# Optimization experiments

Hardware: AMD Instinct MI355X
Metric: run time of the kernel (lower is better)

The kernel has to match this reference:

```python
import jax, jax.numpy as jnp
import numpy as np

B, S, D, H = 4, 2048, 1024, 16
DK = D // H
NEG = -1e9


def setup_inputs() -> dict:
    key = jax.random.key(0)
    ks = jax.random.split(key, 8)
    q = jax.random.normal(ks[0], (B, S, D), dtype=jnp.float32)
    k = jax.random.normal(ks[1], (B, S, D), dtype=jnp.float32)
    v = jax.random.normal(ks[2], (B, S, D), dtype=jnp.float32)
    # causal mask, broadcastable to [B,H,S,S]; mask==0 -> masked out
    mask = jnp.tril(jnp.ones((S, S), dtype=jnp.int32))[None, None, :, :]
    scale = 1.0 / np.sqrt(D)
    w_q = jax.random.normal(ks[3], (D, D), dtype=jnp.float32) * scale
    w_k = jax.random.normal(ks[4], (D, D), dtype=jnp.float32) * scale
    w_v = jax.random.normal(ks[5], (D, D), dtype=jnp.float32) * scale
    w_o = jax.random.normal(ks[6], (D, D), dtype=jnp.float32) * scale
    return {"q": q, "k": k, "v": v, "mask": mask,
            "w_q": w_q, "w_k": w_k, "w_v": w_v, "w_o": w_o}


def reference(q, k, v, mask, w_q, w_k, w_v, w_o):
    # projections (nn.Linear with no bias: x @ W^T)
    def proj(x, w):
        y = jnp.einsum('bsd,ed->bse', x, w)          # [B,S,D]
        return y.reshape(B, -1, H, DK).transpose(0, 2, 1, 3)  # [B,H,S,DK]
    Q, K, V = proj(q, w_q), proj(k, w_k), proj(v, w_v)
    scores = jnp.einsum('bhqd,bhkd->bhqk', Q, K) * (DK ** -0.5)  # [B,H,S,S]
    scores = jnp.where(mask == 0, NEG, scores)
    attn = jax.nn.softmax(scores, axis=-1)
    x = jnp.einsum('bhqk,bhkd->bhqd', attn, V)       # [B,H,S,DK]
    x = x.transpose(0, 2, 1, 3).reshape(B, -1, D)    # [B,S,D]
    return jnp.einsum('bsd,ed->bse', x, w_o)
```

## Files before the change

kernel.cpp:

```cpp
#include <hip/hip_runtime.h>
#include <hip/hip_bf16.h>
#include <stdint.h>

#define B_ 4
#define S_ 2048
#define D_ 1024
#define H_ 16
#define DK_ 64

typedef __hip_bfloat16 bf16;
typedef __attribute__((ext_vector_type(8))) __bf16 bf16x8;
typedef __attribute__((ext_vector_type(4))) __bf16 bf16x4;
typedef __attribute__((ext_vector_type(4))) float f32x4;
typedef __attribute__((ext_vector_type(4))) uint32_t u32x4;

#define QSCALE 0.18033688011112042f

#if defined(__has_builtin)
#if __has_builtin(__builtin_amdgcn_exp2f)
#define EXP2(x) __builtin_amdgcn_exp2f(x)
#endif
#endif
#ifndef EXP2
#define EXP2(x) exp2f(x)
#endif

__device__ __forceinline__ void async_copy16(const void* g, void* l) {
    __builtin_amdgcn_global_load_lds((const __attribute__((address_space(1))) void*)g,
                                     (__attribute__((address_space(3))) void*)l,
                                     16, 0, 0);
}

__device__ __forceinline__ bf16x8 ld8(const bf16* p) {
    return *(const bf16x8*)p;
}

__device__ __forceinline__ uint32_t pk2(float a, float b) {
    union { __bf16 h; uint16_t u; } x, y;
    x.h = (__bf16)a; y.h = (__bf16)b;
    return (uint32_t)x.u | ((uint32_t)y.u << 16);
}

__device__ __forceinline__ bf16x8 cvt8(float4 u0, float4 u1) {
    return (bf16x8){(__bf16)u0.x, (__bf16)u0.y, (__bf16)u0.z, (__bf16)u0.w,
                    (__bf16)u1.x, (__bf16)u1.y, (__bf16)u1.z, (__bf16)u1.w};
}

__device__ __forceinline__ bf16x8 transpose_p(const float* p0, const float* p1,
                                              int srcl, bool loT) {
    uint32_t x0 = pk2(p0[0], p0[1]), x1 = pk2(p0[2], p0[3]);
    uint32_t y0 = pk2(p1[0], p1[1]), y1 = pk2(p1[2], p1[3]);
    u32x4 dw;
#pragma unroll
    for (int i = 0; i < 4; i++) {
        int sl = srcl + (i >> 1) * 16;
        uint32_t vA = (uint32_t)__shfl((int)((i & 1) ? x1 : x0), sl, 64);
        uint32_t vB = (uint32_t)__shfl((int)((i & 1) ? y1 : y0), sl, 64);
        dw[i] = loT ? vA : vB;
    }
    return __builtin_bit_cast(bf16x8, dw);
}

__global__ __launch_bounds__(256) void cvtw(const float4* __restrict__ s0,
                                            const float4* __restrict__ s1,
                                            const float4* __restrict__ s2,
                                            const float4* __restrict__ s3,
                                            bf16x4* __restrict__ d0,
                                            bf16x4* __restrict__ d1,
                                            bf16x4* __restrict__ d2,
                                            bf16x4* __restrict__ d3) {
    int i = blockIdx.x * 256 + threadIdx.x;
    int seg = i >> 18;
    int j   = i & 262143;
    const float4* s = seg == 0 ? s0 : seg == 1 ? s1 : seg == 2 ? s2 : s3;
    bf16x4*       d = seg == 0 ? d0 : seg == 1 ? d1 : seg == 2 ? d2 : d3;
    float4 f = s[j];
    d[j] = (bf16x4){(__bf16)f.x, (__bf16)f.y, (__bf16)f.z, (__bf16)f.w};
}

__global__ __launch_bounds__(256) void cvtx(const float* __restrict__ s0,
                                            const float* __restrict__ s1,
                                            const float* __restrict__ s2,
                                            bf16* __restrict__ d0,
                                            bf16* __restrict__ d1,
                                            bf16* __restrict__ d2) {
    const int z = blockIdx.z;
    const float* s = z == 0 ? s0 : z == 1 ? s1 : s2;
    bf16*        d = z == 0 ? d0 : z == 1 ? d1 : d2;
    size_t i = ((size_t)blockIdx.x * 256 + threadIdx.x) * 8;
    float4 u0 = *(const float4*)(s + i);
    float4 u1 = *(const float4*)(s + i + 4);
    *(bf16x8*)(d + i) = cvt8(u0, u1);
}

__global__ __launch_bounds__(256) void gemm_qkv_bf(const bf16* __restrict__ Aq,
                                                   const bf16* __restrict__ Ak,
                                                   const bf16* __restrict__ Av,
                                                   const bf16* __restrict__ Wqb,
                                                   const bf16* __restrict__ Wkb,
                                                   const bf16* __restrict__ Wvb,
                                                   bf16* __restrict__ Oq,
                                                   bf16* __restrict__ Ok,
                                                   bf16* __restrict__ Ov) {
    __shared__ bf16 lA[128 * 32];
    __shared__ bf16 lW[128 * 32];
    const int z = blockIdx.z;
    const bf16* A = z == 0 ? Aq : z == 1 ? Ak : Av;
    const bf16* W = z == 0 ? Wqb : z == 1 ? Wkb : Wvb;
    bf16*      out = z == 0 ? Oq : z == 1 ? Ok : Ov;

    const int tid  = threadIdx.x;
    const int lane = tid & 63;
    const int quad = lane >> 4;
    const int lo   = lane & 15;
    const int wave = tid >> 6;
    const int wm   = (wave >> 1) * 64;
    const int wn   = (wave & 1) * 64;
    const int n0   = blockIdx.y * 128;
    const int m0   = blockIdx.x * 128;
    const int K    = 1024;

    f32x4 acc[4][4];
#pragma unroll
    for (int i = 0; i < 4; i++)
#pragma unroll
        for (int j = 0; j < 4; j++) acc[i][j] = (f32x4){0.f, 0.f, 0.f, 0.f};

    const int sr = tid >> 2;
    const int sc = (tid & 3) * 8;

    for (int k0 = 0; k0 < K; k0 += 32) {
        async_copy16(A + (size_t)(m0 + sr) * K + k0 + sc,       lA + sr * 32 + sc);
        async_copy16(A + (size_t)(m0 + 64 + sr) * K + k0 + sc,  lA + (64 + sr) * 32 + sc);
        async_copy16(W + (size_t)(n0 + sr) * K + k0 + sc,       lW + sr * 32 + sc);
        async_copy16(W + (size_t)(n0 + 64 + sr) * K + k0 + sc,  lW + (64 + sr) * 32 + sc);
        __syncthreads();

        bf16x8 af[4], bfr[4];
#pragma unroll
        for (int i = 0; i < 4; i++)
            af[i] = ld8(lA + (wm + i * 16 + lo) * 32 + quad * 8);
#pragma unroll
        for (int j = 0; j < 4; j++)
            bfr[j] = ld8(lW + (wn + j * 16 + lo) * 32 + quad * 8);
#pragma unroll
        for (int i = 0; i < 4; i++)
#pragma unroll
            for (int j = 0; j < 4; j++)
                acc[i][j] = __builtin_amdgcn_mfma_f32_16x16x32_bf16(af[i], bfr[j], acc[i][j], 0, 0, 0);
        __syncthreads();
    }

#pragma unroll
    for (int i = 0; i < 4; i++)
#pragma unroll
        for (int j = 0; j < 4; j++)
#pragma unroll
            for (int r = 0; r < 4; r++) {
                int m = m0 + wm + i * 16 + quad * 4 + r;
                int n = n0 + wn + j * 16 + lo;
                float val = acc[i][j][r];
                int b = m >> 11, s = m & (S_ - 1);
                int h = n >> 6, dk = n & 63;
                if (z == 0) {
                    out[((size_t)(b * H_ + h) * S_ + s) * DK_ + dk] =
                        __float2bfloat16(val * QSCALE);
                } else if (z == 1) {
                    out[((size_t)(b * H_ + h) * S_ + s) * DK_ + dk] = __float2bfloat16(val);
                } else {
                    out[((size_t)(b * H_ + h) * DK_ + dk) * S_ + s] = __float2bfloat16(val);
                }
            }
}

__global__ __launch_bounds__(256) void gemm_qkv(const float* __restrict__ Aq,
                                                const float* __restrict__ Ak,
                                                const float* __restrict__ Av,
                                                const bf16* __restrict__ Wqb,
                                                const bf16* __restrict__ Wkb,
                                                const bf16* __restrict__ Wvb,
                                                bf16* __restrict__ Oq,
                                                bf16* __restrict__ Ok,
                                                bf16* __restrict__ Ov) {
    __shared__ bf16 lA[128 * 32];
    __shared__ bf16 lW[128 * 32];
    const int z = blockIdx.z;
    const float* A = z == 0 ? Aq : z == 1 ? Ak : Av;
    const bf16*  W = z == 0 ? Wqb : z == 1 ? Wkb : Wvb;
    bf16*      out = z == 0 ? Oq : z == 1 ? Ok : Ov;

    const int tid  = threadIdx.x;
    const int lane = tid & 63;
    const int quad = lane >> 4;
    const int lo   = lane & 15;
    const int wave = tid >> 6;
    const int wm   = (wave >> 1) * 64;
    const int wn   = (wave & 1) * 64;
    const int n0   = blockIdx.y * 128;
    const int m0   = blockIdx.x * 128;
    const int K    = 1024;

    f32x4 acc[4][4];
#pragma unroll
    for (int i = 0; i < 4; i++)
#pragma unroll
        for (int j = 0; j < 4; j++) acc[i][j] = (f32x4){0.f, 0.f, 0.f, 0.f};

    const int sr = tid >> 2;
    const int sc = (tid & 3) * 8;

    for (int k0 = 0; k0 < K; k0 += 32) {
        async_copy16(W + (size_t)(n0 + sr) * K + k0 + sc,       lW + sr * 32 + sc);
        async_copy16(W + (size_t)(n0 + 64 + sr) * K + k0 + sc,  lW + (64 + sr) * 32 + sc);
        const float* a0 = A + (size_t)(m0 + sr) * K + k0 + sc;
        const float* a1 = A + (size_t)(m0 + 64 + sr) * K + k0 + sc;
        float4 u0 = *(const float4*)a0;
        float4 u1 = *(const float4*)(a0 + 4);
        float4 u2 = *(const float4*)a1;
        float4 u3 = *(const float4*)(a1 + 4);
        *(bf16x8*)(lA + sr * 32 + sc)        = cvt8(u0, u1);
        *(bf16x8*)(lA + (64 + sr) * 32 + sc) = cvt8(u2, u3);
        __syncthreads();

        bf16x8 af[4], bfr[4];
#pragma unroll
        for (int i = 0; i < 4; i++)
            af[i] = ld8(lA + (wm + i * 16 + lo) * 32 + quad * 8);
#pragma unroll
        for (int j = 0; j < 4; j++)
            bfr[j] = ld8(lW + (wn + j * 16 + lo) * 32 + quad * 8);
#pragma unroll
        for (int i = 0; i < 4; i++)
#pragma unroll
            for (int j = 0; j < 4; j++)
                acc[i][j] = __builtin_amdgcn_mfma_f32_16x16x32_bf16(af[i], bfr[j], acc[i][j], 0, 0, 0);
        __syncthreads();
    }

#pragma unroll
    for (int i = 0; i < 4; i++)
#pragma unroll
        for (int j = 0; j < 4; j++)
#pragma unroll
            for (int r = 0; r < 4; r++) {
                int m = m0 + wm + i * 16 + quad * 4 + r;
                int n = n0 + wn + j * 16 + lo;
                float val = acc[i][j][r];
                int b = m >> 11, s = m & (S_ - 1);
                int h = n >> 6, dk = n & 63;
                if (z == 0) {
                    out[((size_t)(b * H_ + h) * S_ + s) * DK_ + dk] =
                        __float2bfloat16(val * QSCALE);
                } else if (z == 1) {
                    out[((size_t)(b * H_ + h) * S_ + s) * DK_ + dk] = __float2bfloat16(val);
                } else {
                    out[((size_t)(b * H_ + h) * DK_ + dk) * S_ + s] = __float2bfloat16(val);
                }
            }
}

__global__ __launch_bounds__(256) void gemm_out(const bf16* __restrict__ A,
                                                const bf16* __restrict__ W,
                                                float* __restrict__ out) {
    __shared__ bf16 lA[128 * 32];
    __shared__ bf16 lW[128 * 32];
    const int tid  = threadIdx.x;
    const int lane = tid & 63;
    const int quad = lane >> 4;
    const int lo   = lane & 15;
    const int wave = tid >> 6;
    const int wm   = (wave >> 1) * 64;
    const int wn   = (wave & 1) * 64;
    const int n0   = blockIdx.y * 128;
    const int m0   = blockIdx.x * 128;
    const int K    = 1024;

    f32x4 acc[4][4];
#pragma unroll
    for (int i = 0; i < 4; i++)
#pragma unroll
        for (int j = 0; j < 4; j++) acc[i][j] = (f32x4){0.f, 0.f, 0.f, 0.f};

    const int sr = tid >> 2;
    const int sc = (tid & 3) * 8;

    for (int k0 = 0; k0 < K; k0 += 32) {
        async_copy16(A + (size_t)(m0 + sr) * K + k0 + sc,       lA + sr * 32 + sc);
        async_copy16(A + (size_t)(m0 + 64 + sr) * K + k0 + sc,  lA + (64 + sr) * 32 + sc);
        async_copy16(W + (size_t)(n0 + sr) * K + k0 + sc,       lW + sr * 32 + sc);
        async_copy16(W + (size_t)(n0 + 64 + sr) * K + k0 + sc,  lW + (64 + sr) * 32 + sc);
        __syncthreads();

        bf16x8 af[4], bfr[4];
#pragma unroll
        for (int i = 0; i < 4; i++)
            af[i] = ld8(lA + (wm + i * 16 + lo) * 32 + quad * 8);
#pragma unroll
        for (int j = 0; j < 4; j++)
            bfr[j] = ld8(lW + (wn + j * 16 + lo) * 32 + quad * 8);
#pragma unroll
        for (int i = 0; i < 4; i++)
#pragma unroll
            for (int j = 0; j < 4; j++)
                acc[i][j] = __builtin_amdgcn_mfma_f32_16x16x32_bf16(af[i], bfr[j], acc[i][j], 0, 0, 0);
        __syncthreads();
    }

#pragma unroll
    for (int i = 0; i < 4; i++)
#pragma unroll
        for (int j = 0; j < 4; j++)
#pragma unroll
            for (int r = 0; r < 4; r++) {
                int m = m0 + wm + i * 16 + quad * 4 + r;
                int n = n0 + wn + j * 16 + lo;
                out[(size_t)m * D_ + n] = acc[i][j][r];
            }
}

__global__ __launch_bounds__(128) void attn(const bf16* __restrict__ Q,
                                            const bf16* __restrict__ K,
                                            const bf16* __restrict__ Vt,
                                            bf16* __restrict__ X) {
    __shared__ f32x4 sO[4][4][64];
    __shared__ float sL[4][64];
    const int tid  = threadIdx.x;
    const int wid  = tid >> 6;
    const int lane = tid & 63;
    const int quad = lane >> 4;
    const int lo   = lane & 15;
    const int idx  = blockIdx.x;
    const int bh   = idx & 63;
    const int qbp  = 31 - (idx >> 6);
    const int q0   = qbp * 64;

    const bf16* Qp = Q  + (size_t)bh * S_ * DK_;
    const bf16* Kp = K  + (size_t)bh * S_ * DK_;
    const bf16* Vp = Vt + (size_t)bh * DK_ * S_;

    bf16x8 bQ[4][2];
#pragma unroll
    for (int qs = 0; qs < 4; qs++) {
        const bf16* qp = Qp + (size_t)(q0 + qs * 16 + lo) * DK_ + quad * 8;
        bQ[qs][0] = ld8(qp);
        bQ[qs][1] = ld8(qp + 32);
    }

    f32x4 out[4][4];
    float lsum[4] = {0.f, 0.f, 0.f, 0.f};
#pragma unroll
    for (int qs = 0; qs < 4; qs++)
#pragma unroll
        for (int t = 0; t < 4; t++) out[qs][t] = (f32x4){0.f, 0.f, 0.f, 0.f};

    const int NT   = 2 * qbp + 2;
    const int half = NT >> 1;
    const int it0  = wid * half;
    const int it1  = it0 + half;
    const int srcl = (quad & 1) * 32 + lo;
    const bool loT = (quad < 2);

    bf16x8 aK0, aK1, aK2, aK3;
    {
        const bf16* kn = Kp + (size_t)(it0 * 32 + lo) * DK_ + quad * 8;
        aK0 = ld8(kn); aK1 = ld8(kn + 32);
        aK2 = ld8(kn + 16 * DK_); aK3 = ld8(kn + 16 * DK_ + 32);
    }

    for (int it = it0; it < it1; ++it) {
        const int kv0 = it * 32;
        const int am = (it < 2 * qbp) ? 0 : (it == 2 * qbp ? 1 : 2);
        const int bm = (it < 2 * qbp + 1) ? 0 : 1;

        bf16x8 aV[4];
#pragma unroll
        for (int t = 0; t < 4; t++)
            aV[t] = ld8(Vp + (size_t)(t * 16 + lo) * S_ + kv0 + quad * 8);

        f32x4 st[4][2];
        __builtin_amdgcn_s_setprio(1);
#pragma unroll
        for (int qs = 0; qs < 4; qs++) {
            f32x4 t0 = (f32x4){0.f, 0.f, 0.f, 0.f};
            f32x4 t1 = (f32x4){0.f, 0.f, 0.f, 0.f};
            t0 = __builtin_amdgcn_mfma_f32_16x16x32_bf16(aK0, bQ[qs][0], t0, 0, 0, 0);
            t0 = __builtin_amdgcn_mfma_f32_16x16x32_bf16(aK1, bQ[qs][1], t0, 0, 0, 0);
            t1 = __builtin_amdgcn_mfma_f32_16x16x32_bf16(aK2, bQ[qs][0], t1, 0, 0, 0);
            t1 = __builtin_amdgcn_mfma_f32_16x16x32_bf16(aK3, bQ[qs][1], t1, 0, 0, 0);
            st[qs][0] = t0; st[qs][1] = t1;
        }
        __builtin_amdgcn_s_setprio(0);

        {
            int kvn = it + 1; if (kvn >= it1) kvn = it1 - 1;
            const bf16* kn = Kp + (size_t)(kvn * 32 + lo) * DK_ + quad * 8;
            aK0 = ld8(kn); aK1 = ld8(kn + 32);
            aK2 = ld8(kn + 16 * DK_); aK3 = ld8(kn + 16 * DK_ + 32);
        }

        bf16x8 bP[4];
#pragma unroll
        for (int pr = 0; pr < 2; pr++) {
            const int mode = pr == 0 ? am : bm;
            const int sl = pr * 2, sh = pr * 2 + 1;
            float pl0[4], pl1[4], ph0[4], ph1[4];
#pragma unroll
            for (int r = 0; r < 4; r++) {
                float el0 = EXP2(st[sl][0][r]);
                float el1 = EXP2(st[sl][1][r]);
                float eh0 = EXP2(st[sh][0][r]);
                float eh1 = EXP2(st[sh][1][r]);
                if (mode == 1) {
                    bool c = (quad * 4 + r) <= lo;
                    el0 = c ? el0 : 0.f;
                    el1 = 0.f;
                    eh1 = c ? eh1 : 0.f;
                } else if (mode == 2) {
                    el0 = 0.f; el1 = 0.f; eh0 = 0.f; eh1 = 0.f;
                }
                pl0[r] = el0; pl1[r] = el1; ph0[r] = eh0; ph1[r] = eh1;
                lsum[sl] += el0 + el1;
                lsum[sh] += eh0 + eh1;
            }
            bP[sl] = transpose_p(pl0, pl1, srcl, loT);
            bP[sh] = transpose_p(ph0, ph1, srcl, loT);
        }

        __builtin_amdgcn_s_setprio(1);
#pragma unroll
        for (int qs = 0; qs < 4; qs++)
#pragma unroll
            for (int t = 0; t < 4; t++)
                out[qs][t] = __builtin_amdgcn_mfma_f32_16x16x32_bf16(aV[t], bP[qs], out[qs][t], 0, 0, 0);
        __builtin_amdgcn_s_setprio(0);
    }

    if (wid == 1) {
#pragma unroll
        for (int qs = 0; qs < 4; qs++) {
#pragma unroll
            for (int t = 0; t < 4; t++) sO[qs][t][lane] = out[qs][t];
            sL[qs][lane] = lsum[qs];
        }
    }
    __syncthreads();
    if (wid == 0) {
        const int b = bh >> 4, h = bh & 15;
#pragma unroll
        for (int qs = 0; qs < 4; qs++) {
#pragma unroll
            for (int t = 0; t < 4; t++) {
                f32x4 p = sO[qs][t][lane];
                out[qs][t][0] += p[0]; out[qs][t][1] += p[1];
                out[qs][t][2] += p[2]; out[qs][t][3] += p[3];
            }
            float ls = lsum[qs] + sL[qs][lane];
            ls += __shfl_xor(ls, 16, 64);
            ls += __shfl_xor(ls, 32, 64);
            const float rl = 1.f / ls;
            bf16* Xp = X + (size_t)(b * S_ + q0 + qs * 16 + lo) * D_ + h * 64;
#pragma unroll
            for (int t = 0; t < 4; t++) {
                uint32_t* d = (uint32_t*)(Xp + t * 16 + quad * 4);
                d[0] = pk2(out[qs][t][0] * rl, out[qs][t][1] * rl);
                d[1] = pk2(out[qs][t][2] * rl, out[qs][t][3] * rl);
            }
        }
    }
}

extern "C" void kernel_launch(void* const* d_in, const int* in_sizes, int n_in,
                              void* d_out, int out_size, void* d_ws, size_t ws_size,
                              hipStream_t stream) {
    const float* q  = (const float*)d_in[0];
    const float* k  = (const float*)d_in[1];
    const float* v  = (const float*)d_in[2];
    const float* wq = (const float*)d_in[4];
    const float* wk = (const float*)d_in[5];
    const float* wv = (const float*)d_in[6];
    const float* wo = (const float*)d_in[7];

    const size_t elems  = (size_t)B_ * S_ * D_;
    const size_t welems = (size_t)D_ * D_;
    bf16* WoB = (bf16*)d_ws;
    bf16* WqB = WoB + welems;
    bf16* WkB = WqB + welems;
    bf16* WvB = WkB + welems;
    bf16* Xb  = WqB;
    bf16* Qw  = WqB + elems;
    bf16* Kw  = Qw + elems;
    bf16* Vw  = Kw + elems;
    bf16* Aqb = Vw + elems;
    bf16* Akb = Aqb + elems;
    bf16* Avb = Akb + elems;

    const size_t need_big = ((size_t)(Avb + elems) - (size_t)d_ws);

    hipLaunchKernelGGL(cvtw, dim3(4 * (int)(welems / 4) / 256), dim3(256), 0, stream,
                       (const float4*)wq, (const float4*)wk, (const float4*)wv,
                       (const float4*)wo,
                       (bf16x4*)WqB, (bf16x4*)WkB, (bf16x4*)WvB, (bf16x4*)WoB);

    if (ws_size >= need_big) {
        hipLaunchKernelGGL(cvtx, dim3((int)(elems / 8 / 256), 1, 3), dim3(256), 0, stream,
                           q, k, v, Aqb, Akb, Avb);
        hipLaunchKernelGGL(gemm_qkv_bf, dim3((B_ * S_) / 128, D_ / 128, 3), dim3(256), 0,
                           stream, Aqb, Akb, Avb, WqB, WkB, WvB, Qw, Kw, Vw);
    } else {
        hipLaunchKernelGGL(gemm_qkv, dim3((B_ * S_) / 128, D_ / 128, 3), dim3(256), 0,
                           stream, q, k, v, WqB, WkB, WvB, Qw, Kw, Vw);
    }

    hipLaunchKernelGGL(attn, dim3((S_ / 64) * B_ * H_), dim3(128), 0, stream, Qw, Kw, Vw, Xb);
    hipLaunchKernelGGL(gemm_out, dim3((B_ * S_) / 128, D_ / 128), dim3(256), 0, stream,
                       Xb, WoB, (float*)d_out);
}
```

Measured before the change: 344.8 us.

## Double-buffer LDS tiles in projection GEMMs to overlap global loads with MFMA

Both the QKV projection GEMM and the output projection GEMM now use two LDS buffers. The async copy of the next K-slice is issued before computing on the current one, with explicit waitcnt and barrier placement and one barrier per iteration instead of two. The MFMA block is wrapped in s_setprio to favour the compute wave. This is meant to hide global-to-LDS latency in GEMMs that were previously fully serialized. In exchange, LDS use per block doubles, which could reduce occupancy.

```diff
diff --git a/kernel.cpp b/kernel.cpp
--- a/kernel.cpp
+++ b/kernel.cpp
@@ -102,8 +102,8 @@
                                                    bf16* __restrict__ Oq,
                                                    bf16* __restrict__ Ok,
                                                    bf16* __restrict__ Ov) {
-    __shared__ bf16 lA[128 * 32];
-    __shared__ bf16 lW[128 * 32];
+    __shared__ bf16 lA[2][128 * 32];
+    __shared__ bf16 lW[2][128 * 32];
     const int z = blockIdx.z;
     const bf16* A = z == 0 ? Aq : z == 1 ? Ak : Av;
     const bf16* W = z == 0 ? Wqb : z == 1 ? Wkb : Wvb;
@@ -129,26 +129,49 @@
     const int sr = tid >> 2;
     const int sc = (tid & 3) * 8;
 
-    for (int k0 = 0; k0 < K; k0 += 32) {
-        async_copy16(A + (size_t)(m0 + sr) * K + k0 + sc,       lA + sr * 32 + sc);
-        async_copy16(A + (size_t)(m0 + 64 + sr) * K + k0 + sc,  lA + (64 + sr) * 32 + sc);
-        async_copy16(W + (size_t)(n0 + sr) * K + k0 + sc,       lW + sr * 32 + sc);
-        async_copy16(W + (size_t)(n0 + 64 + sr) * K + k0 + sc,  lW + (64 + sr) * 32 + sc);
-        __syncthreads();
+    async_copy16(A + (size_t)(m0 + sr) * K + sc,       lA[0] + sr * 32 + sc);
+    async_copy16(A + (size_t)(m0 + 64 + sr) * K + sc,  lA[0] + (64 + sr) * 32 + sc);
+    async_copy16(W + (size_t)(n0 + sr) * K + sc,       lW[0] + sr * 32 + sc);
+    async_copy16(W + (size_t)(n0 + 64 + sr) * K + sc,  lW[0] + (64 + sr) * 32 + sc);
+    asm volatile("s_waitcnt vmcnt(0)" ::: "memory");
+    __builtin_amdgcn_s_barrier();
+    __builtin_amdgcn_sched_barrier(0);
+
+    for (int t = 0; t < 32; ++t) {
+        const int cur = t & 1;
+        bf16* cA = lA[cur];
+        bf16* cW = lW[cur];
+        if (t < 31) {
+            const int kn = (t + 1) * 32;
+            bf16* nA = lA[cur ^ 1];
+            bf16* nW = lW[cur ^ 1];
+            async_copy16(A + (size_t)(m0 + sr) * K + kn + sc,       nA + sr * 32 + sc);
+            async_copy16(A + (size_t)(m0 + 64 + sr) * K + kn + sc,  nA + (64 + sr) * 32 + sc);
+            async_copy16(W + (size_t)(n0 + sr) * K + kn + sc,       nW + sr * 32 + sc);
+            async_copy16(W + (size_t)(n0 + 64 + sr) * K + kn + sc,  nW + (64 + sr) * 32 + sc);
+        }
 
         bf16x8 af[4], bfr[4];
 #pragma unroll
         for (int i = 0; i < 4; i++)
-            af[i] = ld8(lA + (wm + i * 16 + lo) * 32 + quad * 8);
+            af[i] = ld8(cA + (wm + i * 16 + lo) * 32 + quad * 8);
 #pragma unroll
         for (int j = 0; j < 4; j++)
-            bfr[j] = ld8(lW + (wn + j * 16 + lo) * 32 + quad * 8);
+            bfr[j] = ld8(cW + (wn + j * 16 + lo) * 32 + quad * 8);
+        asm volatile("s_waitcnt lgkmcnt(0)" ::: "memory");
+        __builtin_amdgcn_sched_barrier(0);
+
+        __builtin_amdgcn_s_setprio(1);
 #pragma unroll
         for (int i = 0; i < 4; i++)
 #pragma unroll
             for (int j = 0; j < 4; j++)
                 acc[i][j] = __builtin_amdgcn_mfma_f32_16x16x32_bf16(af[i], bfr[j], acc[i][j], 0, 0, 0);
-        __syncthreads();
+        __builtin_amdgcn_s_setprio(0);
+
+        asm volatile("s_waitcnt vmcnt(0)" ::: "memory");
+        __builtin_amdgcn_s_barrier();
+        __builtin_amdgcn_sched_barrier(0);
     }
 
 #pragma unroll
@@ -262,8 +285,8 @@
 __global__ __launch_bounds__(256) void gemm_out(const bf16* __restrict__ A,
                                                 const bf16* __restrict__ W,
                                                 float* __restrict__ out) {
-    __shared__ bf16 lA[128 * 32];
-    __shared__ bf16 lW[128 * 32];
+    __shared__ bf16 lA[2][128 * 32];
+    __shared__ bf16 lW[2][128 * 32];
     const int tid  = threadIdx.x;
     const int lane = tid & 63;
     const int quad = lane >> 4;
@@ -284,26 +307,49 @@
     const int sr = tid >> 2;
     const int sc = (tid & 3) * 8;
 
-    for (int k0 = 0; k0 < K; k0 += 32) {
-        async_copy16(A + (size_t)(m0 + sr) * K + k0 + sc,       lA + sr * 32 + sc);
-        async_copy16(A + (size_t)(m0 + 64 + sr) * K + k0 + sc,  lA + (64 + sr) * 32 + sc);
-        async_copy16(W + (size_t)(n0 + sr) * K + k0 + sc,       lW + sr * 32 + sc);
-        async_copy16(W + (size_t)(n0 + 64 + sr) * K + k0 + sc,  lW + (64 + sr) * 32 + sc);
-        __syncthreads();
+    async_copy16(A + (size_t)(m0 + sr) * K + sc,       lA[0] + sr * 32 + sc);
+    async_copy16(A + (size_t)(m0 + 64 + sr) * K + sc,  lA[0] + (64 + sr) * 32 + sc);
+    async_copy16(W + (size_t)(n0 + sr) * K + sc,       lW[0] + sr * 32 + sc);
+    async_copy16(W + (size_t)(n0 + 64 + sr) * K + sc,  lW[0] + (64 + sr) * 32 + sc);
+    asm volatile("s_waitcnt vmcnt(0)" ::: "memory");
+    __builtin_amdgcn_s_barrier();
+    __builtin_amdgcn_sched_barrier(0);
+
+    for (int t = 0; t < 32; ++t) {
+        const int cur = t & 1;
+        bf16* cA = lA[cur];
+        bf16* cW = lW[cur];
+        if (t < 31) {
+            const int kn = (t + 1) * 32;
+            bf16* nA = lA[cur ^ 1];
+            bf16* nW = lW[cur ^ 1];
+            async_copy16(A + (size_t)(m0 + sr) * K + kn + sc,       nA + sr * 32 + sc);
+            async_copy16(A + (size_t)(m0 + 64 + sr) * K + kn + sc,  nA + (64 + sr) * 32 + sc);
+            async_copy16(W + (size_t)(n0 + sr) * K + kn + sc,       nW + sr * 32 + sc);
+            async_copy16(W + (size_t)(n0 + 64 + sr) * K + kn + sc,  nW + (64 + sr) * 32 + sc);
+        }
 
         bf16x8 af[4], bfr[4];
 #pragma unroll
         for (int i = 0; i < 4; i++)
-            af[i] = ld8(lA + (wm + i * 16 + lo) * 32 + quad * 8);
+            af[i] = ld8(cA + (wm + i * 16 + lo) * 32 + quad * 8);
 #pragma unroll
         for (int j = 0; j < 4; j++)
-            bfr[j] = ld8(lW + (wn + j * 16 + lo) * 32 + quad * 8);
+            bfr[j] = ld8(cW + (wn + j * 16 + lo) * 32 + quad * 8);
+        asm volatile("s_waitcnt lgkmcnt(0)" ::: "memory");
+        __builtin_amdgcn_sched_barrier(0);
+
+        __builtin_amdgcn_s_setprio(1);
 #pragma unroll
         for (int i = 0; i < 4; i++)
 #pragma unroll
             for (int j = 0; j < 4; j++)
                 acc[i][j] = __builtin_amdgcn_mfma_f32_16x16x32_bf16(af[i], bfr[j], acc[i][j], 0, 0, 0);
-        __syncthreads();
+        __builtin_amdgcn_s_setprio(0);
+
+        asm volatile("s_waitcnt vmcnt(0)" ::: "memory");
+        __builtin_amdgcn_s_barrier();
+        __builtin_amdgcn_sched_barrier(0);
     }
 
 #pragma unroll
```

Measured after the change: 342.8 us. About the same (-0.6%).

## Double-buffer GEMM LDS tiles with 64-wide K and XOR swizzle

Applied to the files above, without the earlier changes.

Both projection GEMMs (fused QKV and output) now stage 128x64 A and W tiles into double-buffered LDS. The next K tile is prefetched with async global-to-LDS copies while MFMAs run on the current tile, and there is one barrier per iteration instead of two. An XOR swizzle on the column index is meant to avoid LDS bank conflicts on the fragment reads. In exchange, LDS use per block grows to 64KB, which may limit how many blocks fit on a CU.

```diff
diff --git a/kernel.cpp b/kernel.cpp
--- a/kernel.cpp
+++ b/kernel.cpp
@@ -44,6 +44,17 @@
 __device__ __forceinline__ bf16x8 cvt8(float4 u0, float4 u1) {
     return (bf16x8){(__bf16)u0.x, (__bf16)u0.y, (__bf16)u0.z, (__bf16)u0.w,
                     (__bf16)u1.x, (__bf16)u1.y, (__bf16)u1.z, (__bf16)u1.w};
+}
+
+__device__ __forceinline__ void stage_tile(const bf16* __restrict__ g, int ldg,
+                                           bf16* l, int tid) {
+#pragma unroll
+    for (int i = 0; i < 4; i++) {
+        int row = i * 32 + (tid >> 3);
+        int ce  = (tid & 7) * 8;
+        int cs  = ce ^ ((row & 7) << 3);
+        async_copy16(g + (size_t)row * ldg + cs, l + row * 64 + ce);
+    }
 }
 
 __device__ __forceinline__ bf16x8 transpose_p(const float* p0, const float* p1,
@@ -102,8 +113,8 @@
                                                    bf16* __restrict__ Oq,
                                                    bf16* __restrict__ Ok,
                                                    bf16* __restrict__ Ov) {
-    __shared__ bf16 lA[128 * 32];
-    __shared__ bf16 lW[128 * 32];
+    __shared__ bf16 lA[2][128 * 64];
+    __shared__ bf16 lW[2][128 * 64];
     const int z = blockIdx.z;
     const bf16* A = z == 0 ? Aq : z == 1 ? Ak : Av;
     const bf16* W = z == 0 ? Wqb : z == 1 ? Wkb : Wvb;
@@ -119,6 +130,7 @@
     const int n0   = blockIdx.y * 128;
     const int m0   = blockIdx.x * 128;
     const int K    = 1024;
+    const int swz  = (lo & 7) << 3;
 
     f32x4 acc[4][4];
 #pragma unroll
@@ -126,29 +138,35 @@
 #pragma unroll
         for (int j = 0; j < 4; j++) acc[i][j] = (f32x4){0.f, 0.f, 0.f, 0.f};
 
-    const int sr = tid >> 2;
-    const int sc = (tid & 3) * 8;
-
-    for (int k0 = 0; k0 < K; k0 += 32) {
-        async_copy16(A + (size_t)(m0 + sr) * K + k0 + sc,       lA + sr * 32 + sc);
-        async_copy16(A + (size_t)(m0 + 64 + sr) * K + k0 + sc,  lA + (64 + sr) * 32 + sc);
-        async_copy16(W + (size_t)(n0 + sr) * K + k0 + sc,       lW + sr * 32 + sc);
-        async_copy16(W + (size_t)(n0 + 64 + sr) * K + k0 + sc,  lW + (64 + sr) * 32 + sc);
-        __syncthreads();
-
-        bf16x8 af[4], bfr[4];
-#pragma unroll
-        for (int i = 0; i < 4; i++)
-            af[i] = ld8(lA + (wm + i * 16 + lo) * 32 + quad * 8);
-#pragma unroll
-        for (int j = 0; j < 4; j++)
-            bfr[j] = ld8(lW + (wn + j * 16 + lo) * 32 + quad * 8);
-#pragma unroll
-        for (int i = 0; i < 4; i++)
+    stage_tile(A + (size_t)m0 * K, K, lA[0], tid);
+    stage_tile(W + (size_t)n0 * K, K, lW[0], tid);
+
+    for (int t = 0; t < 16; ++t) {
+        const int cur = t & 1;
+        asm volatile("s_waitcnt vmcnt(0)" ::: "memory");
+        __builtin_amdgcn_s_barrier();
+        if (t < 15) {
+            const int kn = (t + 1) * 64;
+            stage_tile(A + (size_t)m0 * K + kn, K, lA[cur ^ 1], tid);
+            stage_tile(W + (size_t)n0 * K + kn, K, lW[cur ^ 1], tid);
+        }
+        const bf16* cA = lA[cur];
+        const bf16* cW = lW[cur];
+#pragma unroll
+        for (int ks = 0; ks < 2; ks++) {
+            bf16x8 af[4], bfr[4];
+#pragma unroll
+            for (int i = 0; i < 4; i++)
+                af[i] = ld8(cA + (wm + i * 16 + lo) * 64 + ((ks * 32 + quad * 8) ^ swz));
 #pragma unroll
             for (int j = 0; j < 4; j++)
-                acc[i][j] = __builtin_amdgcn_mfma_f32_16x16x32_bf16(af[i], bfr[j], acc[i][j], 0, 0, 0);
-        __syncthreads();
+                bfr[j] = ld8(cW + (wn + j * 16 + lo) * 64 + ((ks * 32 + quad * 8) ^ swz));
+#pragma unroll
+            for (int i = 0; i < 4; i++)
+#pragma unroll
+                for (int j = 0; j < 4; j++)
+                    acc[i][j] = __builtin_amdgcn_mfma_f32_16x16x32_bf16(af[i], bfr[j], acc[i][j], 0, 0, 0);
+        }
     }
 
 #pragma unroll
@@ -262,8 +280,8 @@
 __global__ __launch_bounds__(256) void gemm_out(const bf16* __restrict__ A,
                                                 const bf16* __restrict__ W,
                                                 float* __restrict__ out) {
-    __shared__ bf16 lA[128 * 32];
-    __shared__ bf16 lW[128 * 32];
+    __shared__ bf16 lA[2][128 * 64];
+    __shared__ bf16 lW[2][128 * 64];
     const int tid  = threadIdx.x;
     const int lane = tid & 63;
     const int quad = lane >> 4;
@@ -274,6 +292,7 @@
     const int n0   = blockIdx.y * 128;
     const int m0   = blockIdx.x * 128;
     const int K    = 1024;
+    const int swz  = (lo & 7) << 3;
 
     f32x4 acc[4][4];
 #pragma unroll
@@ -281,29 +300,35 @@
 #pragma unroll
         for (int j = 0; j < 4; j++) acc[i][j] = (f32x4){0.f, 0.f, 0.f, 0.f};
 
-    const int sr = tid >> 2;
-    const int sc = (tid & 3) * 8;
-
-    for (int k0 = 0; k0 < K; k0 += 32) {
-        async_copy16(A + (size_t)(m0 + sr) * K + k0 + sc,       lA + sr * 32 + sc);
-        async_copy16(A + (size_t)(m0 + 64 + sr) * K + k0 + sc,  lA + (64 + sr) * 32 + sc);
-        async_copy16(W + (size_t)(n0 + sr) * K + k0 + sc,       lW + sr * 32 + sc);
-        async_copy16(W + (size_t)(n0 + 64 + sr) * K + k0 + sc,  lW + (64 + sr) * 32 + sc);
-        __syncthreads();
-
-        bf16x8 af[4], bfr[4];
-#pragma unroll
-        for (int i = 0; i < 4; i++)
-            af[i] = ld8(lA + (wm + i * 16 + lo) * 32 + quad * 8);
-#pragma unroll
-        for (int j = 0; j < 4; j++)
-            bfr[j] = ld8(lW + (wn + j * 16 + lo) * 32 + quad * 8);
-#pragma unroll
-        for (int i = 0; i < 4; i++)
+    stage_tile(A + (size_t)m0 * K, K, lA[0], tid);
+    stage_tile(W + (size_t)n0 * K, K, lW[0], tid);
+
+    for (int t = 0; t < 16; ++t) {
+        const int cur = t & 1;
+        asm volatile("s_waitcnt vmcnt(0)" ::: "memory");
+        __builtin_amdgcn_s_barrier();
+        if (t < 15) {
+            const int kn = (t + 1) * 64;
+            stage_tile(A + (size_t)m0 * K + kn, K, lA[cur ^ 1], tid);
+            stage_tile(W + (size_t)n0 * K + kn, K, lW[cur ^ 1], tid);
+        }
+        const bf16* cA = lA[cur];
+        const bf16* cW = lW[cur];
+#pragma unroll
+        for (int ks = 0; ks < 2; ks++) {
+            bf16x8 af[4], bfr[4];
+#pragma unroll
+            for (int i = 0; i < 4; i++)
+                af[i] = ld8(cA + (wm + i * 16 + lo) * 64 + ((ks * 32 + quad * 8) ^ swz));
 #pragma unroll
             for (int j = 0; j < 4; j++)
-                acc[i][j] = __builtin_amdgcn_mfma_f32_16x16x32_bf16(af[i], bfr[j], acc[i][j], 0, 0, 0);
-        __syncthreads();
+                bfr[j] = ld8(cW + (wn + j * 16 + lo) * 64 + ((ks * 32 + quad * 8) ^ swz));
+#pragma unroll
+            for (int i = 0; i < 4; i++)
+#pragma unroll
+                for (int j = 0; j < 4; j++)
+                    acc[i][j] = __builtin_amdgcn_mfma_f32_16x16x32_bf16(af[i], bfr[j], acc[i][j], 0, 0, 0);
+        }
     }
 
 #pragma unroll
```

After: 351.6 us. Within noise of the previous version (+2.0%).
